# Optimization experiments

Measured on AMD Instinct MI355X. Metric: run time of the kernel, lower is better.

## Reference

```python
import jax, jax.numpy as jnp
import numpy as np
import math

B, S, D, H = 4, 2048, 768, 12
DK = D // H

def setup_inputs() -> dict:
    key = jax.random.key(0)
    ks = jax.random.split(key, 12)
    sc = 1.0 / math.sqrt(D)
    return {
        'Q': jax.random.normal(ks[0], (B, S, D), jnp.float32),
        'K': jax.random.normal(ks[1], (B, S, D), jnp.float32),
        'V': jax.random.normal(ks[2], (B, S, D), jnp.float32),
        'mask': jax.random.randint(ks[3], (B, 1, S, S), 0, 2, jnp.int32),
        'Wq': jax.random.normal(ks[4], (D, D), jnp.float32) * sc,
        'bq': jnp.zeros((D,), jnp.float32),
        'Wk': jax.random.normal(ks[5], (D, D), jnp.float32) * sc,
        'bk': jnp.zeros((D,), jnp.float32),
        'Wv': jax.random.normal(ks[6], (D, D), jnp.float32) * sc,
        'bv': jnp.zeros((D,), jnp.float32),
        'Wo': jax.random.normal(ks[7], (D, D), jnp.float32) * sc,
        'bo': jnp.zeros((D,), jnp.float32),
    }

def _split_heads(x):
    # [B,S,D] -> [B,H,S,DK]
    return x.reshape(B, S, H, DK).transpose(0, 2, 1, 3)

def reference(Q, K, V, mask, Wq, bq, Wk, bk, Wv, bv, Wo, bo):
    q = _split_heads(Q @ Wq.T + bq)
    k = _split_heads(K @ Wk.T + bk)
    v = _split_heads(V @ Wv.T + bv)
    scores = jnp.einsum('bhqd,bhkd->bhqk', q, k) / math.sqrt(DK)
    # Faithful to the source: masked positions are filled with -1e-9 (NOT -inf)
    scores = jnp.where(mask == 0, jnp.float32(-1e-9), scores)
    attn = jax.nn.softmax(scores, axis=-1)
    x = jnp.einsum('bhqk,bhkd->bhqd', attn, v)          # [B,H,S,DK]
    x = x.transpose(0, 2, 1, 3).reshape(B, S, D)         # [B,S,D]
    return x @ Wo.T + bo
```

## Files before the change

### kernel.cpp

```cpp
#include <hip/hip_runtime.h>

#define BB 4
#define SS 2048
#define DD 768
#define HH 12
#define DKK 64
#define MM (BB*SS)

typedef __attribute__((ext_vector_type(8))) short bf16x8;
typedef __attribute__((ext_vector_type(4))) float f32x4;

#define GLDS(g, l) __builtin_amdgcn_global_load_lds( \
    (const __attribute__((address_space(1))) unsigned int*)(g), \
    (__attribute__((address_space(3))) unsigned int*)(l), 16, 0, 0)

__device__ __forceinline__ unsigned short f2bf(float f) {
    union { float f; unsigned int u; } v; v.f = f;
    unsigned int r = v.u + 0x7fffu + ((v.u >> 16) & 1u);
    return (unsigned short)(r >> 16);
}

#define EXPSCALE 0.18033688011112042f

#define ABLK2 (MM*DD/4/512)
#define WBLK2 (DD*DD/4/512)
#define MBLK2 (BB*SS*SS/1024)
#define SEGW  (3*ABLK2)
#define SEGM  (SEGW + 4*WBLK2)

__global__ void prep(
    const float* __restrict__ Q, const float* __restrict__ K, const float* __restrict__ V,
    const float* __restrict__ Wq, const float* __restrict__ Wk, const float* __restrict__ Wv,
    const float* __restrict__ Wo, const int* __restrict__ mask,
    unsigned short* __restrict__ Qc, unsigned short* __restrict__ Kc, unsigned short* __restrict__ Vc,
    unsigned short* __restrict__ Wqc, unsigned short* __restrict__ Wkc, unsigned short* __restrict__ Wvc,
    unsigned short* __restrict__ Woc, unsigned int* __restrict__ mbits)
{
    const int bx = blockIdx.x;
    if (bx < SEGW) {
        const int seg = bx / ABLK2;
        const float* s = seg == 0 ? Q : seg == 1 ? K : V;
        unsigned short* d = seg == 0 ? Qc : seg == 1 ? Kc : Vc;
        const int i0 = (bx - seg * ABLK2) * 512 + threadIdx.x;
        #pragma unroll
        for (int j = 0; j < 2; j++) {
            const int i = i0 + j * 256;
            float4 v = ((const float4*)s)[i];
            ushort4 o;
            o.x = f2bf(v.x); o.y = f2bf(v.y); o.z = f2bf(v.z); o.w = f2bf(v.w);
            ((ushort4*)d)[i] = o;
        }
    } else if (bx < SEGM) {
        const int b2 = bx - SEGW;
        const int seg = b2 / WBLK2;
        const float* s = seg == 0 ? Wq : seg == 1 ? Wk : seg == 2 ? Wv : Wo;
        unsigned short* d = seg == 0 ? Wqc : seg == 1 ? Wkc : seg == 2 ? Wvc : Woc;
        const int i0 = (b2 - seg * WBLK2) * 512 + threadIdx.x;
        #pragma unroll
        for (int j = 0; j < 2; j++) {
            const int i = i0 + j * 256;
            float4 v = ((const float4*)s)[i];
            ushort4 o;
            o.x = f2bf(v.x); o.y = f2bf(v.y); o.z = f2bf(v.z); o.w = f2bf(v.w);
            ((ushort4*)d)[i] = o;
        }
    } else {
        const int blk = bx - SEGM;
        const int chunk = blk * 4 + (threadIdx.x >> 6);
        const int l = threadIdx.x & 63;
        const int4 mv = *(const int4*)(mask + (size_t)chunk * 256 + 4 * l);
        const unsigned int nib = (mv.x != 0 ? 1u : 0u) | (mv.y != 0 ? 2u : 0u) |
                                 (mv.z != 0 ? 4u : 0u) | (mv.w != 0 ? 8u : 0u);
        const unsigned long long b0 = __ballot(nib & 1u);
        const unsigned long long b1 = __ballot(nib & 2u);
        const unsigned long long b2 = __ballot(nib & 4u);
        const unsigned long long b3 = __ballot(nib & 8u);
        if (l < 8) {
            const int i = l >> 1;
            const unsigned long long wsel = i == 0 ? b0 : i == 1 ? b1 : i == 2 ? b2 : b3;
            const unsigned int v = (l & 1) ? (unsigned int)(wsel >> 32) : (unsigned int)wsel;
            mbits[(size_t)chunk * 8 + l] = v;
        }
    }
}

__global__ __launch_bounds__(256) void gemm_qkv(
    const unsigned short* __restrict__ Qc, const unsigned short* __restrict__ Kc, const unsigned short* __restrict__ Vc,
    const unsigned short* __restrict__ Wq, const unsigned short* __restrict__ Wk, const unsigned short* __restrict__ Wv,
    const float* __restrict__ bq, const float* __restrict__ bk, const float* __restrict__ bv,
    unsigned short* __restrict__ qb, unsigned short* __restrict__ kb, unsigned short* __restrict__ vt)
{
    __shared__ unsigned short As[128*64];
    __shared__ unsigned short Bs[128*64];
    const int bid = blockIdx.x;
    const int xg  = bid & 7;
    const int s   = bid >> 3;
    const int mat = s / 48;
    const int r   = s % 48;
    const int nb  = r % 6;
    const int mb  = (r / 6) * 8 + xg;
    const int m0 = mb * 128, n0 = nb * 128;

    const unsigned short* X = mat == 0 ? Qc : mat == 1 ? Kc : Vc;
    const unsigned short* W = mat == 0 ? Wq : mat == 1 ? Wk : Wv;
    const float* bias        = mat == 0 ? bq : mat == 1 ? bk : bv;

    const int tid  = threadIdx.x;
    const int lane = tid & 63;
    const int w    = tid >> 6;
    const int wm   = w >> 1, wn = w & 1;
    const int quad = lane >> 4, c = lane & 15;

    f32x4 acc[4][4];
    #pragma unroll
    for (int i = 0; i < 4; i++)
        #pragma unroll
        for (int j = 0; j < 4; j++) acc[i][j] = (f32x4){0.f, 0.f, 0.f, 0.f};

    const unsigned short* Xg[4]; const unsigned short* Wg[4]; int dst[4];
    #pragma unroll
    for (int j = 0; j < 4; j++) {
        const int ch = tid + j * 256;
        const int row = ch >> 3, sl = ch & 7;
        const int lc = (sl ^ (row & 7)) << 3;
        Xg[j] = X + (size_t)(m0 + row) * DD + lc;
        Wg[j] = W + (size_t)(n0 + row) * DD + lc;
        dst[j] = ch * 8;
    }
    const int cswz = c & 7;

    for (int k0 = 0; k0 < DD; k0 += 64) {
        #pragma unroll
        for (int j = 0; j < 4; j++) {
            GLDS(Xg[j] + k0, As + dst[j]);
            GLDS(Wg[j] + k0, Bs + dst[j]);
        }
        __syncthreads();
        #pragma unroll
        for (int kk = 0; kk < 2; kk++) {
            bf16x8 a[4], b[4];
            #pragma unroll
            for (int t = 0; t < 4; t++) {
                const int ra = wm * 64 + t * 16 + c;
                const int rb = wn * 64 + t * 16 + c;
                a[t] = *(const bf16x8*)(As + ra * 64 + (((kk * 4 + quad) ^ cswz) << 3));
                b[t] = *(const bf16x8*)(Bs + rb * 64 + (((kk * 4 + quad) ^ cswz) << 3));
            }
            if (mat < 2) {
                #pragma unroll
                for (int tn = 0; tn < 4; tn++)
                    #pragma unroll
                    for (int tm = 0; tm < 4; tm++)
                        acc[tn][tm] = __builtin_amdgcn_mfma_f32_16x16x32_bf16(b[tn], a[tm], acc[tn][tm], 0, 0, 0);
            } else {
                #pragma unroll
                for (int tm = 0; tm < 4; tm++)
                    #pragma unroll
                    for (int tn = 0; tn < 4; tn++)
                        acc[tm][tn] = __builtin_amdgcn_mfma_f32_16x16x32_bf16(a[tm], b[tn], acc[tm][tn], 0, 0, 0);
            }
        }
        __syncthreads();
    }

    if (mat < 2) {
        unsigned short* out = mat == 0 ? qb : kb;
        const float scale = mat == 0 ? EXPSCALE : 1.0f;
        #pragma unroll
        for (int tn = 0; tn < 4; tn++) {
            const int featbase = n0 + wn * 64 + tn * 16 + quad * 4;
            const float4 bz = *(const float4*)(bias + featbase);
            #pragma unroll
            for (int tm = 0; tm < 4; tm++) {
                const int token = m0 + wm * 64 + tm * 16 + c;
                ushort4 pk;
                pk.x = f2bf((acc[tn][tm][0] + bz.x) * scale);
                pk.y = f2bf((acc[tn][tm][1] + bz.y) * scale);
                pk.z = f2bf((acc[tn][tm][2] + bz.z) * scale);
                pk.w = f2bf((acc[tn][tm][3] + bz.w) * scale);
                *(ushort4*)(out + (size_t)token * DD + featbase) = pk;
            }
        }
    } else {
        #pragma unroll
        for (int tn = 0; tn < 4; tn++) {
            const int col = n0 + wn * 64 + tn * 16 + c;
            const float bz = bias[col];
            const int h = col >> 6, dk = col & 63;
            #pragma unroll
            for (int tm = 0; tm < 4; tm++) {
                const int row = m0 + wm * 64 + tm * 16 + quad * 4;
                const int bb = row >> 11, ss = row & 2047;
                ushort4 pk;
                pk.x = f2bf(acc[tm][tn][0] + bz);
                pk.y = f2bf(acc[tm][tn][1] + bz);
                pk.z = f2bf(acc[tm][tn][2] + bz);
                pk.w = f2bf(acc[tm][tn][3] + bz);
                *(ushort4*)(vt + ((((size_t)bb * HH + h) * DKK + dk) * SS + ss)) = pk;
            }
        }
    }
}

__global__ __launch_bounds__(256, 3) void flash(
    const unsigned short* __restrict__ qb, const unsigned short* __restrict__ kb,
    const unsigned short* __restrict__ vt, const unsigned int* __restrict__ mbits,
    unsigned short* __restrict__ ob)
{
    __shared__ unsigned short Ks[2][64*64];
    __shared__ unsigned short Vs[2][64*64];

    const int bh = blockIdx.y;
    const int bi = bh / HH, h = bh % HH;
    const int tid  = threadIdx.x;
    const int w    = tid >> 6, lane = tid & 63;
    const int quad = lane >> 4, c = lane & 15;
    const int q0w = blockIdx.x * 128 + w * 32;

    bf16x8 qa[2][2];
    #pragma unroll
    for (int mt = 0; mt < 2; mt++) {
        const unsigned short* qbase = qb + (size_t)(bi * SS + q0w + mt * 16 + c) * DD + h * DKK + quad * 8;
        qa[mt][0] = *(const bf16x8*)(qbase);
        qa[mt][1] = *(const bf16x8*)(qbase + 32);
    }

    const int l0 = tid >> 3, sl = tid & 7;
    const int l1 = 32 + l0;
    const int lc = (sl ^ (l0 & 7)) << 3;
    const int kp0 = ((l0 >> 5) << 5) | (((l0 >> 2) & 3) << 3) | (((l0 >> 4) & 1) << 2) | (l0 & 3);
    const int kp1 = ((l1 >> 5) << 5) | (((l1 >> 2) & 3) << 3) | (((l1 >> 4) & 1) << 2) | (l1 & 3);
    const unsigned short* kg0 = kb + ((size_t)bi * SS + kp0) * DD + h * DKK + lc;
    const unsigned short* kg1 = kb + ((size_t)bi * SS + kp1) * DD + h * DKK + lc;
    const unsigned short* vg0 = vt + (((size_t)bi * HH + h) * DKK + l0) * SS + lc;
    const unsigned short* vg1 = vt + (((size_t)bi * HH + h) * DKK + l1) * SS + lc;

    const unsigned int* mr0 = mbits + (size_t)(bi * SS + q0w + c) * 64;
    const unsigned int* mr1 = mr0 + (size_t)16 * 64;

    f32x4 o[2][4];
    #pragma unroll
    for (int mt = 0; mt < 2; mt++)
        #pragma unroll
        for (int dt = 0; dt < 4; dt++) o[mt][dt] = (f32x4){0.f, 0.f, 0.f, 0.f};
    f32x4 osum[2] = { (f32x4){0.f,0.f,0.f,0.f}, (f32x4){0.f,0.f,0.f,0.f} };
    const f32x4 ZC = (f32x4){0.f, 0.f, 0.f, 0.f};
    union { unsigned int u[4]; bf16x8 v; } onesu;
    onesu.u[0] = 0x3F803F80u; onesu.u[1] = 0x3F803F80u;
    onesu.u[2] = 0x3F803F80u; onesu.u[3] = 0x3F803F80u;
    const bf16x8 ones = onesu.v;

    const int cswz = c & 7;

    GLDS(kg0, Ks[0] + (size_t)tid * 8);
    GLDS(kg1, Ks[0] + (size_t)(256 + tid) * 8);
    GLDS(vg0, Vs[0] + (size_t)tid * 8);
    GLDS(vg1, Vs[0] + (size_t)(256 + tid) * 8);

    uint4 wlo[2], whi[2];

    for (int t = 0; t < SS / 64; t++) {
        const int k0 = t * 64, par = t & 1;
        __syncthreads();
        if (t < SS / 64 - 1) {
            const size_t ko = (size_t)(k0 + 64);
            GLDS(kg0 + ko * DD, Ks[par ^ 1] + (size_t)tid * 8);
            GLDS(kg1 + ko * DD, Ks[par ^ 1] + (size_t)(256 + tid) * 8);
            GLDS(vg0 + ko,      Vs[par ^ 1] + (size_t)tid * 8);
            GLDS(vg1 + ko,      Vs[par ^ 1] + (size_t)(256 + tid) * 8);
        }

        if ((t & 3) == 0) {
            const int co = (t >> 2) * 8;
            wlo[0] = *(const uint4*)(mr0 + co);
            whi[0] = *(const uint4*)(mr0 + co + 4);
            wlo[1] = *(const uint4*)(mr1 + co);
            whi[1] = *(const uint4*)(mr1 + co + 4);
        }
        const int t16 = (t & 3) * 16;
        unsigned int ww[2][4];
        #pragma unroll
        for (int mt = 0; mt < 2; mt++) {
            ww[mt][0] = (unsigned int)((((unsigned long long)wlo[mt].y << 32) | wlo[mt].x) >> t16);
            ww[mt][1] = (unsigned int)((((unsigned long long)wlo[mt].w << 32) | wlo[mt].z) >> t16);
            ww[mt][2] = (unsigned int)((((unsigned long long)whi[mt].y << 32) | whi[mt].x) >> t16);
            ww[mt][3] = (unsigned int)((((unsigned long long)whi[mt].w << 32) | whi[mt].z) >> t16);
        }

        #pragma unroll
        for (int p = 0; p < 2; p++) {
            unsigned int pq[2][4];
            #pragma unroll
            for (int tt = 0; tt < 2; tt++) {
                const unsigned short* kbase = &Ks[par][((2 * p + tt) * 16 + c) << 6];
                const bf16x8 kf0 = *(const bf16x8*)(kbase + ((quad ^ cswz) << 3));
                const bf16x8 kf1 = *(const bf16x8*)(kbase + (((4 + quad) ^ cswz) << 3));
                const unsigned int sh = (unsigned)(p * 8 + quad * 2 + tt);
                #pragma unroll
                for (int mt = 0; mt < 2; mt++) {
                    f32x4 st = __builtin_amdgcn_mfma_f32_16x16x32_bf16(kf0, qa[mt][0], ZC, 0, 0, 0);
                    st = __builtin_amdgcn_mfma_f32_16x16x32_bf16(kf1, qa[mt][1], st, 0, 0, 0);
                    #pragma unroll
                    for (int r2 = 0; r2 < 2; r2++) {
                        const float sv0 = ((ww[mt][r2 * 2]     >> sh) & 1u) ? st[r2 * 2]     : 0.0f;
                        const float sv1 = ((ww[mt][r2 * 2 + 1] >> sh) & 1u) ? st[r2 * 2 + 1] : 0.0f;
                        const float p0 = __builtin_amdgcn_exp2f(sv0);
                        const float p1 = __builtin_amdgcn_exp2f(sv1);
                        union { float f; unsigned int u; } u0, u1; u0.f = p0; u1.f = p1;
                        pq[mt][tt * 2 + r2] = __builtin_amdgcn_perm(u1.u, u0.u, 0x07060302);
                    }
                }
            }
            bf16x8 pbv[2];
            #pragma unroll
            for (int mt = 0; mt < 2; mt++) {
                union { unsigned int u[4]; bf16x8 v; } pb;
                pb.u[0] = pq[mt][0]; pb.u[1] = pq[mt][1];
                pb.u[2] = pq[mt][2]; pb.u[3] = pq[mt][3];
                pbv[mt] = pb.v;
                osum[mt] = __builtin_amdgcn_mfma_f32_16x16x32_bf16(ones, pbv[mt], osum[mt], 0, 0, 0);
            }
            #pragma unroll
            for (int dt = 0; dt < 4; dt++) {
                const bf16x8 vf = *(const bf16x8*)(&Vs[par][((dt * 16 + c) << 6) + ((((p << 2) + quad) ^ cswz) << 3)]);
                #pragma unroll
                for (int mt = 0; mt < 2; mt++)
                    o[mt][dt] = __builtin_amdgcn_mfma_f32_16x16x32_bf16(vf, pbv[mt], o[mt][dt], 0, 0, 0);
            }
        }
    }

    #pragma unroll
    for (int mt = 0; mt < 2; mt++) {
        const float rn = __builtin_amdgcn_rcpf(osum[mt][0]);
        unsigned short* op = ob + (size_t)(bi * SS + q0w + mt * 16 + c) * DD + h * DKK + quad * 4;
        #pragma unroll
        for (int dt = 0; dt < 4; dt++) {
            ushort4 pk;
            pk.x = f2bf(o[mt][dt][0] * rn);
            pk.y = f2bf(o[mt][dt][1] * rn);
            pk.z = f2bf(o[mt][dt][2] * rn);
            pk.w = f2bf(o[mt][dt][3] * rn);
            *(ushort4*)(op + dt * 16) = pk;
        }
    }
}

__global__ __launch_bounds__(256) void gemm_out(
    const unsigned short* __restrict__ A, const unsigned short* __restrict__ W,
    const float* __restrict__ bias, float* __restrict__ out)
{
    __shared__ unsigned short As[128*64];
    __shared__ unsigned short Bs[128*64];
    const int bid = blockIdx.x;
    const int xg  = bid & 7;
    const int s   = bid >> 3;
    const int nb  = s % 6;
    const int mb  = (s / 6) * 8 + xg;
    const int m0 = mb * 128, n0 = nb * 128;

    const int tid  = threadIdx.x;
    const int lane = tid & 63;
    const int w    = tid >> 6;
    const int wm   = w >> 1, wn = w & 1;
    const int quad = lane >> 4, c = lane & 15;

    f32x4 acc[4][4];
    #pragma unroll
    for (int i = 0; i < 4; i++)
        #pragma unroll
        for (int j = 0; j < 4; j++) acc[i][j] = (f32x4){0.f, 0.f, 0.f, 0.f};

    const unsigned short* Ag[4]; const unsigned short* Wg[4]; int dst[4];
    #pragma unroll
    for (int j = 0; j < 4; j++) {
        const int ch = tid + j * 256;
        const int row = ch >> 3, sl = ch & 7;
        const int lcc = (sl ^ (row & 7)) << 3;
        Ag[j] = A + (size_t)(m0 + row) * DD + lcc;
        Wg[j] = W + (size_t)(n0 + row) * DD + lcc;
        dst[j] = ch * 8;
    }
    const int cswz = c & 7;

    for (int k0 = 0; k0 < DD; k0 += 64) {
        #pragma unroll
        for (int j = 0; j < 4; j++) {
            GLDS(Ag[j] + k0, As + dst[j]);
            GLDS(Wg[j] + k0, Bs + dst[j]);
        }
        __syncthreads();
        #pragma unroll
        for (int kk = 0; kk < 2; kk++) {
            bf16x8 a[4], b[4];
            #pragma unroll
            for (int t = 0; t < 4; t++) {
                const int ra = wm * 64 + t * 16 + c;
                const int rb = wn * 64 + t * 16 + c;
                a[t] = *(const bf16x8*)(As + ra * 64 + (((kk * 4 + quad) ^ cswz) << 3));
                b[t] = *(const bf16x8*)(Bs + rb * 64 + (((kk * 4 + quad) ^ cswz) << 3));
            }
            #pragma unroll
            for (int tn = 0; tn < 4; tn++)
                #pragma unroll
                for (int tm = 0; tm < 4; tm++)
                    acc[tn][tm] = __builtin_amdgcn_mfma_f32_16x16x32_bf16(b[tn], a[tm], acc[tn][tm], 0, 0, 0);
        }
        __syncthreads();
    }

    #pragma unroll
    for (int tn = 0; tn < 4; tn++) {
        const int featbase = n0 + wn * 64 + tn * 16 + quad * 4;
        const float4 bz = *(const float4*)(bias + featbase);
        #pragma unroll
        for (int tm = 0; tm < 4; tm++) {
            const int token = m0 + wm * 64 + tm * 16 + c;
            float4 v;
            v.x = acc[tn][tm][0] + bz.x;
            v.y = acc[tn][tm][1] + bz.y;
            v.z = acc[tn][tm][2] + bz.z;
            v.w = acc[tn][tm][3] + bz.w;
            *(float4*)(out + (size_t)token * DD + featbase) = v;
        }
    }
}

extern "C" void kernel_launch(void* const* d_in, const int* in_sizes, int n_in,
                              void* d_out, int out_size, void* d_ws, size_t ws_size,
                              hipStream_t stream) {
    (void)in_sizes; (void)n_in; (void)out_size; (void)ws_size;
    const float* Q    = (const float*)d_in[0];
    const float* K    = (const float*)d_in[1];
    const float* V    = (const float*)d_in[2];
    const int*   mask = (const int*)d_in[3];
    const float* Wq   = (const float*)d_in[4];
    const float* bq   = (const float*)d_in[5];
    const float* Wk   = (const float*)d_in[6];
    const float* bk   = (const float*)d_in[7];
    const float* Wv   = (const float*)d_in[8];
    const float* bv   = (const float*)d_in[9];
    const float* Wo   = (const float*)d_in[10];
    const float* bo   = (const float*)d_in[11];
    float* out = (float*)d_out;

    char* ws = (char*)d_ws;
    size_t off = 0;
    auto alloc = [&](size_t bytes) { char* p = ws + off; off += (bytes + 255) & ~255ULL; return p; };
    const size_t act = (size_t)MM * DD * 2;
    unsigned short* Qc  = (unsigned short*)alloc(act);
    unsigned short* Kc  = (unsigned short*)alloc(act);
    unsigned short* Vc  = (unsigned short*)alloc(act);
    unsigned short* Wqc = (unsigned short*)alloc((size_t)DD * DD * 2);
    unsigned short* Wkc = (unsigned short*)alloc((size_t)DD * DD * 2);
    unsigned short* Wvc = (unsigned short*)alloc((size_t)DD * DD * 2);
    unsigned short* Woc = (unsigned short*)alloc((size_t)DD * DD * 2);
    unsigned short* qb  = (unsigned short*)alloc(act);
    unsigned short* kb  = (unsigned short*)alloc(act);
    unsigned short* vt  = (unsigned short*)alloc(act);
    unsigned int*  mbits = (unsigned int*)alloc((size_t)BB * SS * (SS / 32) * 4);
    unsigned short* ob = Qc;

    prep<<<dim3(SEGM + MBLK2), 256, 0, stream>>>(
        Q, K, V, Wq, Wk, Wv, Wo, mask, Qc, Kc, Vc, Wqc, Wkc, Wvc, Woc, mbits);
    gemm_qkv<<<dim3(1152), 256, 0, stream>>>(
        Qc, Kc, Vc, Wqc, Wkc, Wvc, bq, bk, bv, qb, kb, vt);
    flash<<<dim3(SS / 128, BB * HH), 256, 0, stream>>>(qb, kb, vt, mbits, ob);
    gemm_out<<<dim3(384), 256, 0, stream>>>(ob, Woc, bo, out);
}
```

Baseline: 321.5 us.

## Double-buffer LDS tiles in QKV and output projection GEMMs

Both projection GEMMs now use two LDS buffers per operand. The next K-slice is prefetched with global_load_lds into the alternate buffer while MFMAs run on the current one, and the trailing barrier in each iteration is removed. The aim is to hide global-load latency behind matrix math instead of stalling at every k-step. In exchange, LDS use per block doubles to 64 KB, which may lower how many blocks fit per CU.

```diff
diff --git a/kernel.cpp b/kernel.cpp
--- a/kernel.cpp
+++ b/kernel.cpp
@@ -90,8 +90,8 @@
     const float* __restrict__ bq, const float* __restrict__ bk, const float* __restrict__ bv,
     unsigned short* __restrict__ qb, unsigned short* __restrict__ kb, unsigned short* __restrict__ vt)
 {
-    __shared__ unsigned short As[128*64];
-    __shared__ unsigned short Bs[128*64];
+    __shared__ unsigned short As[2][128*64];
+    __shared__ unsigned short Bs[2][128*64];
     const int bid = blockIdx.x;
     const int xg  = bid & 7;
     const int s   = bid >> 3;
@@ -129,13 +129,23 @@
     }
     const int cswz = c & 7;
 
-    for (int k0 = 0; k0 < DD; k0 += 64) {
-        #pragma unroll
-        for (int j = 0; j < 4; j++) {
-            GLDS(Xg[j] + k0, As + dst[j]);
-            GLDS(Wg[j] + k0, Bs + dst[j]);
-        }
+    #pragma unroll
+    for (int j = 0; j < 4; j++) {
+        GLDS(Xg[j], As[0] + dst[j]);
+        GLDS(Wg[j], Bs[0] + dst[j]);
+    }
+
+    for (int it = 0; it < DD / 64; it++) {
+        const int par = it & 1;
         __syncthreads();
+        if (it < DD / 64 - 1) {
+            const int k0 = (it + 1) * 64;
+            #pragma unroll
+            for (int j = 0; j < 4; j++) {
+                GLDS(Xg[j] + k0, As[par ^ 1] + dst[j]);
+                GLDS(Wg[j] + k0, Bs[par ^ 1] + dst[j]);
+            }
+        }
         #pragma unroll
         for (int kk = 0; kk < 2; kk++) {
             bf16x8 a[4], b[4];
@@ -143,8 +153,8 @@
             for (int t = 0; t < 4; t++) {
                 const int ra = wm * 64 + t * 16 + c;
                 const int rb = wn * 64 + t * 16 + c;
-                a[t] = *(const bf16x8*)(As + ra * 64 + (((kk * 4 + quad) ^ cswz) << 3));
-                b[t] = *(const bf16x8*)(Bs + rb * 64 + (((kk * 4 + quad) ^ cswz) << 3));
+                a[t] = *(const bf16x8*)(As[par] + ra * 64 + (((kk * 4 + quad) ^ cswz) << 3));
+                b[t] = *(const bf16x8*)(Bs[par] + rb * 64 + (((kk * 4 + quad) ^ cswz) << 3));
             }
             if (mat < 2) {
                 #pragma unroll
@@ -160,7 +170,6 @@
                         acc[tm][tn] = __builtin_amdgcn_mfma_f32_16x16x32_bf16(a[tm], b[tn], acc[tm][tn], 0, 0, 0);
             }
         }
-        __syncthreads();
     }
 
     if (mat < 2) {
@@ -350,8 +359,8 @@
     const unsigned short* __restrict__ A, const unsigned short* __restrict__ W,
     const float* __restrict__ bias, float* __restrict__ out)
 {
-    __shared__ unsigned short As[128*64];
-    __shared__ unsigned short Bs[128*64];
+    __shared__ unsigned short As[2][128*64];
+    __shared__ unsigned short Bs[2][128*64];
     const int bid = blockIdx.x;
     const int xg  = bid & 7;
     const int s   = bid >> 3;
@@ -383,13 +392,23 @@
     }
     const int cswz = c & 7;
 
-    for (int k0 = 0; k0 < DD; k0 += 64) {
-        #pragma unroll
-        for (int j = 0; j < 4; j++) {
-            GLDS(Ag[j] + k0, As + dst[j]);
-            GLDS(Wg[j] + k0, Bs + dst[j]);
-        }
+    #pragma unroll
+    for (int j = 0; j < 4; j++) {
+        GLDS(Ag[j], As[0] + dst[j]);
+        GLDS(Wg[j], Bs[0] + dst[j]);
+    }
+
+    for (int it = 0; it < DD / 64; it++) {
+        const int par = it & 1;
         __syncthreads();
+        if (it < DD / 64 - 1) {
+            const int k0 = (it + 1) * 64;
+            #pragma unroll
+            for (int j = 0; j < 4; j++) {
+                GLDS(Ag[j] + k0, As[par ^ 1] + dst[j]);
+                GLDS(Wg[j] + k0, Bs[par ^ 1] + dst[j]);
+            }
+        }
         #pragma unroll
         for (int kk = 0; kk < 2; kk++) {
             bf16x8 a[4], b[4];
@@ -397,8 +416,8 @@
             for (int t = 0; t < 4; t++) {
                 const int ra = wm * 64 + t * 16 + c;
                 const int rb = wn * 64 + t * 16 + c;
-                a[t] = *(const bf16x8*)(As + ra * 64 + (((kk * 4 + quad) ^ cswz) << 3));
-                b[t] = *(const bf16x8*)(Bs + rb * 64 + (((kk * 4 + quad) ^ cswz) << 3));
+                a[t] = *(const bf16x8*)(As[par] + ra * 64 + (((kk * 4 + quad) ^ cswz) << 3));
+                b[t] = *(const bf16x8*)(Bs[par] + rb * 64 + (((kk * 4 + quad) ^ cswz) << 3));
             }
             #pragma unroll
             for (int tn = 0; tn < 4; tn++)
@@ -406,7 +425,6 @@
                 for (int tm = 0; tm < 4; tm++)
                     acc[tn][tm] = __builtin_amdgcn_mfma_f32_16x16x32_bf16(b[tn], a[tm], acc[tn][tm], 0, 0, 0);
         }
-        __syncthreads();
     }
 
     #pragma unroll
```

Result: slower. 336.2 us (+4.6%).
